# Kernel optimization log

Measured on AMD Instinct MI355X. Metric: run time of the kernel, lower is better.

Reference implementation:

```python
import jax, jax.numpy as jnp
import numpy as np

H = 8      # head count
ES = 96    # per-head dim
EMB = H * ES
L = 6      # layers
B, T = 8, 512
LN_EPS = 1e-5

def _layernorm(x, g, b):
    mu = jnp.mean(x, axis=-1, keepdims=True)
    var = jnp.mean(jnp.square(x - mu), axis=-1, keepdims=True)
    return (x - mu) * jax.lax.rsqrt(var + LN_EPS) * g + b

def setup_inputs() -> dict:
    key = jax.random.key(0)
    ks = jax.random.split(key, 6)
    s = 0.02
    return {
        "x": jax.random.normal(ks[0], (B, T, EMB), jnp.float32),
        "Wkqv": jax.random.normal(ks[1], (L, 3 * ES, ES), jnp.float32) * s,
        "Wproj": jax.random.normal(ks[2], (L, EMB, EMB), jnp.float32) * s,
        "ln1_g": jnp.ones((L, EMB), jnp.float32),
        "ln1_b": jnp.zeros((L, EMB), jnp.float32),
        "ln2_g": jnp.ones((L, EMB), jnp.float32),
        "ln2_b": jnp.zeros((L, EMB), jnp.float32),
        "ff_w1": jax.random.normal(ks[3], (L, 4 * EMB, EMB), jnp.float32) * s,
        "ff_b1": jnp.zeros((L, 4 * EMB), jnp.float32),
        "ff_w2": jax.random.normal(ks[4], (L, EMB, 4 * EMB), jnp.float32) * s,
        "ff_b2": jnp.zeros((L, EMB), jnp.float32),
    }

def _forward(x, Wkqv, Wproj, ln1_g, ln1_b, ln2_g, ln2_b, ff_w1, ff_b1, ff_w2, ff_b2):
    scale = 1.0 / jnp.sqrt(jnp.float32(ES))

    def step(carry, p):
        x, prev = carry
        wkqv, wproj, g1, b1, g2, b2, w1, bb1, w2, bb2 = p
        Bx, Tx, _ = x.shape
        xh = x.reshape(Bx, Tx, H, ES)                         # [B,T,H,es]
        kqv = jnp.einsum('bthe,fe->bthf', xh, wkqv)           # [B,T,H,3es]
        k, q, v = jnp.split(kqv, 3, axis=-1)                  # torch.split order: k,q,v
        # residual attention: raw scores + previous layer's raw scores
        score = jnp.einsum('bihk,bjhk->bijh', q, k) * scale + prev  # [B,T,T,H]
        att = jax.nn.softmax(score, axis=2)                   # over key axis j
        res = jnp.einsum('btih,bihs->bths', att, v).reshape(Bx, Tx, EMB)
        res = res @ wproj.T
        x = _layernorm(x + res, g1, b1)
        ff = jax.nn.gelu(x @ w1.T + bb1, approximate=False) @ w2.T + bb2
        x = _layernorm(x + ff, g2, b2)
        return (x, score), None

    prev0 = jnp.zeros((x.shape[0], x.shape[1], x.shape[1], H), x.dtype)
    (x, _), _ = jax.lax.scan(step, (x, prev0),
                             (Wkqv, Wproj, ln1_g, ln1_b, ln2_g, ln2_b,
                              ff_w1, ff_b1, ff_w2, ff_b2))
    return x

def reference(x, Wkqv, Wproj, ln1_g, ln1_b, ln2_g, ln2_b, ff_w1, ff_b1, ff_w2, ff_b2):
    return _forward(x, Wkqv, Wproj, ln1_g, ln1_b, ln2_g, ln2_b, ff_w1, ff_b1, ff_w2, ff_b2)
```

## Files before the change

kernel.cpp:

```cpp
#include <hip/hip_runtime.h>
#include <math.h>

#define BB 8
#define TT 512
#define HH 8
#define ESS 96
#define EMBD 768
#define FFD 3072
#define NLAYER 6
#define KHMAX 576

typedef unsigned short ushort_t;
typedef __attribute__((ext_vector_type(8))) short short8;
typedef __attribute__((ext_vector_type(4))) float f32x4;
typedef __attribute__((ext_vector_type(4))) unsigned short ushort4v;

static __device__ __forceinline__ ushort_t f2b(float f) {
    unsigned u = __builtin_bit_cast(unsigned, f);
    unsigned r = (u + 0x7fffu + ((u >> 16) & 1u)) >> 16;
    return (ushort_t)r;
}
static __device__ __forceinline__ float b2f(ushort_t u) {
    return __builtin_bit_cast(float, ((unsigned)u) << 16);
}

#define GLDS(gp, lp) __builtin_amdgcn_global_load_lds( \
    (const __attribute__((address_space(1))) void*)(gp), \
    (__attribute__((address_space(3))) void*)(lp), 16, 0, 0)

template<int BM, int BN, int WM, int WN, int OUTBF, int HASBIAS, int GELU, int BETA>
__global__ __launch_bounds__(256) void gemm_mfma(
    const ushort_t* __restrict__ A, int lda,
    const ushort_t* __restrict__ B, int ldb,
    void* __restrict__ Cv, int ldc,
    int K, float alpha,
    const float* __restrict__ bias,
    int bdiv, long sAb, long sAh, long sBb, long sBh, long sCb, long sCh)
{
    constexpr int BK = 32;
    constexpr int WTM = BM / WM;
    constexpr int WTN = BN / WN;
    constexpr int MF = WTM / 16, NF = WTN / 16;
    constexpr int ACH = (BM * BK * 2) / 1024;
    constexpr int BCH = (BN * BK * 2) / 1024;

    const int z = blockIdx.z;
    const int zb = z / bdiv, zh = z % bdiv;
    A += (long)zb * sAb + (long)zh * sAh;
    B += (long)zb * sBb + (long)zh * sBh;
    const long coff = (long)zb * sCb + (long)zh * sCh;

    __shared__ ushort_t As[BM * BK];
    __shared__ ushort_t Bs[BN * BK];

    const int tid = threadIdx.x;
    const int w = tid >> 6, lane = tid & 63;
    const int wr = w / WN, wc = w % WN;
    const int m0 = blockIdx.y * BM;
    const int n0 = blockIdx.x * BN;

    f32x4 acc[MF][NF] = {};

    const int fr = lane & 15;
    const int kb = lane >> 4;

    for (int k0 = 0; k0 < K; k0 += BK) {
#pragma unroll
        for (int q = 0; q < (ACH + 3) / 4; ++q) {
            int ci = q * 4 + w;
            if (ci < ACH) {
                int e = ci * 512 + lane * 8;
                int r = e >> 5, c = e & 31;
                GLDS(A + (long)(m0 + r) * lda + (k0 + c), (char*)As + ci * 1024);
            }
        }
#pragma unroll
        for (int q = 0; q < (BCH + 3) / 4; ++q) {
            int ci = q * 4 + w;
            if (ci < BCH) {
                int e = ci * 512 + lane * 8;
                int r = e >> 5, c = e & 31;
                GLDS(B + (long)(n0 + r) * ldb + (k0 + c), (char*)Bs + ci * 1024);
            }
        }
        __syncthreads();

        short8 af[MF], bfr[NF];
#pragma unroll
        for (int fm = 0; fm < MF; ++fm)
            af[fm] = *(const short8*)&As[(wr * WTM + fm * 16 + fr) * 32 + kb * 8];
#pragma unroll
        for (int fn = 0; fn < NF; ++fn)
            bfr[fn] = *(const short8*)&Bs[(wc * WTN + fn * 16 + fr) * 32 + kb * 8];
#pragma unroll
        for (int fm = 0; fm < MF; ++fm)
#pragma unroll
            for (int fn = 0; fn < NF; ++fn)
                acc[fm][fn] = __builtin_amdgcn_mfma_f32_16x16x32_bf16(
                    af[fm], bfr[fn], acc[fm][fn], 0, 0, 0);
        __syncthreads();
    }

    const int cr = lane >> 4;
    const int cc = lane & 15;
#pragma unroll
    for (int fm = 0; fm < MF; ++fm) {
#pragma unroll
        for (int fn = 0; fn < NF; ++fn) {
#pragma unroll
            for (int j = 0; j < 4; ++j) {
                int gm = m0 + wr * WTM + fm * 16 + cr * 4 + j;
                int gn = n0 + wc * WTN + fn * 16 + cc;
                float v = alpha * acc[fm][fn][j];
                if (HASBIAS) v += bias[gn];
                if (GELU) {
                    float zz = 1.5957691216f * fmaf(0.044715f * v * v, v, v);
                    v = v / (1.f + __expf(-zz));
                }
                long idx = coff + (long)gm * ldc + gn;
                if (BETA) v += ((const float*)Cv)[idx];
                if (OUTBF) ((ushort_t*)Cv)[idx] = f2b(v);
                else       ((float*)Cv)[idx] = v;
            }
        }
    }
}

__global__ __launch_bounds__(256) void kqv_gemm(
    const ushort_t* __restrict__ A,
    const ushort_t* __restrict__ Bw,
    ushort_t* __restrict__ Kh, ushort_t* __restrict__ Qh,
    ushort_t* __restrict__ Vt, int loff, float scale)
{
    constexpr int BM = 128, BN = 96, BK = 32;
    __shared__ ushort_t As[BM * BK];
    __shared__ ushort_t Bs[BN * BK];

    const int tid = threadIdx.x;
    const int w = tid >> 6, lane = tid & 63;
    const int m0 = blockIdx.y * BM;
    const int n0 = blockIdx.x * BN;

    f32x4 acc[2][6] = {};
    const int fr = lane & 15;
    const int kb = lane >> 4;

    for (int k0 = 0; k0 < 96; k0 += BK) {
#pragma unroll
        for (int q = 0; q < 2; ++q) {
            int ci = q * 4 + w;
            int e = ci * 512 + lane * 8;
            int r = e >> 5, c = e & 31;
            GLDS(A + (long)(m0 + r) * ESS + (k0 + c), (char*)As + ci * 1024);
        }
        {
            int ci = w;
            int e = ci * 512 + lane * 8;
            int r = e >> 5, c = e & 31;
            GLDS(Bw + (long)(n0 + r) * ESS + (k0 + c), (char*)Bs + ci * 1024);
            if (w < 2) {
                int ci2 = 4 + w;
                int e2 = ci2 * 512 + lane * 8;
                int r2 = e2 >> 5, c2 = e2 & 31;
                GLDS(Bw + (long)(n0 + r2) * ESS + (k0 + c2), (char*)Bs + ci2 * 1024);
            }
        }
        __syncthreads();

        short8 af[2], bfr[6];
#pragma unroll
        for (int fm = 0; fm < 2; ++fm)
            af[fm] = *(const short8*)&As[(w * 32 + fm * 16 + fr) * 32 + kb * 8];
#pragma unroll
        for (int fn = 0; fn < 6; ++fn)
            bfr[fn] = *(const short8*)&Bs[(fn * 16 + fr) * 32 + kb * 8];
#pragma unroll
        for (int fm = 0; fm < 2; ++fm)
#pragma unroll
            for (int fn = 0; fn < 6; ++fn)
                acc[fm][fn] = __builtin_amdgcn_mfma_f32_16x16x32_bf16(
                    af[fm], bfr[fn], acc[fm][fn], 0, 0, 0);
        __syncthreads();
    }

    const int cr = lane >> 4;
    const int cc = lane & 15;
    const int kind = blockIdx.x;
#pragma unroll
    for (int fm = 0; fm < 2; ++fm) {
#pragma unroll
        for (int fn = 0; fn < 6; ++fn) {
#pragma unroll
            for (int j = 0; j < 4; ++j) {
                int gm = m0 + w * 32 + fm * 16 + cr * 4 + j;
                int s = fn * 16 + cc;
                float v = acc[fm][fn][j];
                int h = gm & 7;
                int bt = gm >> 3;
                int t = bt & 511, b = bt >> 9;
                int bh = b * HH + h;
                if (kind == 0)
                    Kh[((long)(bh * TT + t)) * KHMAX + loff + s] = f2b(v);
                else if (kind == 1)
                    Qh[((long)(bh * TT + t)) * KHMAX + loff + s] = f2b(v * scale);
                else
                    Vt[((long)(bh * ESS + s)) * TT + t] = f2b(v);
            }
        }
    }
}

__global__ __launch_bounds__(256) void fused_attn(
    const ushort_t* __restrict__ Qh,
    const ushort_t* __restrict__ Kh,
    const ushort_t* __restrict__ Vt,
    ushort_t* __restrict__ attn,
    int Kd)
{
    __shared__ char lds[40960];
    ushort_t* As = (ushort_t*)lds;
    ushort_t* Bs = (ushort_t*)(lds + 2048);
    ushort_t* Pt = (ushort_t*)(lds + 2048);
    ushort_t* Vs = (ushort_t*)(lds + 34816);
    float* red   = (float*)(lds + 34816);
    float* red2  = (float*)(lds + 35328);

    const int wg = blockIdx.x;
    const int xcd = wg & 7;
    const int sub = wg >> 3;
    const int m0 = (sub & 15) * 32;
    const int bh = (sub >> 4) * 8 + xcd;
    const int b = bh >> 3, h = bh & 7;

    const int tid = threadIdx.x;
    const int w = tid >> 6, lane = tid & 63;
    const int fr = lane & 15, kb = lane >> 4;
    const int cr = kb, cc = fr;

    f32x4 acc[2][8] = {};

    for (int k0 = 0; k0 < Kd; k0 += 32) {
        if (w < 2) {
            int e = w * 512 + lane * 8;
            int r = e >> 5, c = e & 31;
            GLDS(Qh + ((long)(bh * TT + m0 + r)) * KHMAX + k0 + c,
                 (char*)As + w * 1024);
        }
#pragma unroll
        for (int q = 0; q < 8; ++q) {
            int ci = q * 4 + w;
            int e = ci * 512 + lane * 8;
            int r = e >> 5, c = e & 31;
            GLDS(Kh + ((long)(bh * TT + r)) * KHMAX + k0 + c,
                 (char*)Bs + ci * 1024);
        }
        __syncthreads();
        short8 af0 = *(const short8*)&As[fr * 32 + kb * 8];
        short8 af1 = *(const short8*)&As[(16 + fr) * 32 + kb * 8];
#pragma unroll
        for (int fn = 0; fn < 8; ++fn) {
            short8 bf = *(const short8*)&Bs[(w * 128 + fn * 16 + fr) * 32 + kb * 8];
            acc[0][fn] = __builtin_amdgcn_mfma_f32_16x16x32_bf16(af0, bf, acc[0][fn], 0, 0, 0);
            acc[1][fn] = __builtin_amdgcn_mfma_f32_16x16x32_bf16(af1, bf, acc[1][fn], 0, 0, 0);
        }
        __syncthreads();
    }

#pragma unroll
    for (int fm = 0; fm < 2; ++fm)
#pragma unroll
        for (int j = 0; j < 4; ++j) {
            float mx = -1e30f;
#pragma unroll
            for (int fn = 0; fn < 8; ++fn) mx = fmaxf(mx, acc[fm][fn][j]);
            for (int o = 1; o <= 8; o <<= 1) mx = fmaxf(mx, __shfl_xor(mx, o));
            if (cc == 0) red[w * 32 + fm * 16 + cr * 4 + j] = mx;
        }
    __syncthreads();

    float inv[2][4];
#pragma unroll
    for (int fm = 0; fm < 2; ++fm)
#pragma unroll
        for (int j = 0; j < 4; ++j) {
            int r = fm * 16 + cr * 4 + j;
            float mx = fmaxf(fmaxf(red[r], red[32 + r]), fmaxf(red[64 + r], red[96 + r]));
            float s = 0.f;
#pragma unroll
            for (int fn = 0; fn < 8; ++fn) {
                float e = __expf(acc[fm][fn][j] - mx);
                acc[fm][fn][j] = e;
                s += e;
            }
            for (int o = 1; o <= 8; o <<= 1) s += __shfl_xor(s, o);
            if (cc == 0) red2[w * 32 + r] = s;
        }
    __syncthreads();
#pragma unroll
    for (int fm = 0; fm < 2; ++fm)
#pragma unroll
        for (int j = 0; j < 4; ++j) {
            int r = fm * 16 + cr * 4 + j;
            inv[fm][j] = 1.f / (red2[r] + red2[32 + r] + red2[64 + r] + red2[96 + r]);
        }

#pragma unroll
    for (int fm = 0; fm < 2; ++fm)
#pragma unroll
        for (int fn = 0; fn < 8; ++fn)
#pragma unroll
            for (int j = 0; j < 4; ++j) {
                int row = fm * 16 + cr * 4 + j;
                int col = w * 128 + fn * 16 + cc;
                Pt[row * 512 + (col ^ ((row & 7) << 3))] = f2b(acc[fm][fn][j] * inv[fm][j]);
            }
    __syncthreads();

    const int wr = w >> 1, wc2 = w & 1;
    f32x4 po[3] = {};
    for (int j0 = 0; j0 < TT; j0 += 32) {
#pragma unroll
        for (int q = 0; q < 2; ++q) {
            int ci = q * 4 + w;
            if (ci < 6) {
                int e = ci * 512 + lane * 8;
                int r = e >> 5, c = e & 31;
                GLDS(Vt + ((long)(bh * ESS + r)) * TT + j0 + c, (char*)Vs + ci * 1024);
            }
        }
        __syncthreads();
        int prow = wr * 16 + fr;
        short8 pa = *(const short8*)&Pt[prow * 512 + ((j0 + kb * 8) ^ ((prow & 7) << 3))];
#pragma unroll
        for (int fn = 0; fn < 3; ++fn) {
            short8 vb = *(const short8*)&Vs[(wc2 * 48 + fn * 16 + fr) * 32 + kb * 8];
            po[fn] = __builtin_amdgcn_mfma_f32_16x16x32_bf16(pa, vb, po[fn], 0, 0, 0);
        }
        __syncthreads();
    }

#pragma unroll
    for (int fn = 0; fn < 3; ++fn)
#pragma unroll
        for (int j = 0; j < 4; ++j) {
            int grow = m0 + wr * 16 + cr * 4 + j;
            int gcol = h * ESS + wc2 * 48 + fn * 16 + cc;
            attn[((long)(b * TT + grow)) * EMBD + gcol] = f2b(po[fn][j]);
        }
}

__global__ __launch_bounds__(256) void cvt_f2b(
    const float* __restrict__ in, ushort_t* __restrict__ out)
{
    const int i = blockIdx.x * 256 + threadIdx.x;
    float4 v = ((const float4*)in)[i];
    ushort4v o = {f2b(v.x), f2b(v.y), f2b(v.z), f2b(v.w)};
    ((ushort4v*)out)[i] = o;
}

static __device__ __forceinline__ void cvt_w_one(
    int r, int layer,
    const float* Wkqv, const float* Wproj, const float* w1, const float* w2,
    ushort_t* dst_layer)
{
    const float* src; int base;
    if (r < 6912)        { src = Wkqv  + (long)layer * 27648;   base = 0; }
    else if (r < 154368) { src = Wproj + (long)layer * 589824;  base = 6912; }
    else if (r < 744192) { src = w1    + (long)layer * 2359296; base = 154368; }
    else                 { src = w2    + (long)layer * 2359296; base = 744192; }
    int j = r - base;
    float4 v = ((const float4*)src)[j];
    ushort4v o = {f2b(v.x), f2b(v.y), f2b(v.z), f2b(v.w)};
    ((ushort4v*)dst_layer)[r] = o;
}

__global__ __launch_bounds__(256) void cvt_weights_all(
    const float* __restrict__ Wkqv, const float* __restrict__ Wproj,
    const float* __restrict__ w1, const float* __restrict__ w2,
    ushort_t* __restrict__ dst)
{
    int i4 = blockIdx.x * 256 + threadIdx.x;
    int layer = i4 / 1334016;
    int r = i4 - layer * 1334016;
    cvt_w_one(r, layer, Wkqv, Wproj, w1, w2, dst + (long)layer * 5336064);
}

__global__ __launch_bounds__(256) void cvt_weights_layer(
    const float* __restrict__ Wkqv, const float* __restrict__ Wproj,
    const float* __restrict__ w1, const float* __restrict__ w2,
    ushort_t* __restrict__ dst, int layer)
{
    int r = blockIdx.x * 256 + threadIdx.x;
    cvt_w_one(r, layer, Wkqv, Wproj, w1, w2, dst);
}

__global__ __launch_bounds__(192) void add_ln(
    float* __restrict__ x, const ushort_t* __restrict__ r0,
    const ushort_t* __restrict__ r1, const float* __restrict__ bias,
    const float* __restrict__ g, const float* __restrict__ bta,
    ushort_t* __restrict__ xb)
{
    const long row = blockIdx.x;
    float4* xr = (float4*)(x + row * EMBD);
    const ushort4v* q0 = (const ushort4v*)(r0 + row * EMBD);
    const ushort4v* q1 = (const ushort4v*)(r1 + row * EMBD);
    __shared__ float sh[4];
    const int tid = threadIdx.x;
    const int lane = tid & 63, w = tid >> 6;

    float4 a = xr[tid];
    ushort4v u0 = q0[tid], u1 = q1[tid];
    float v[4] = {a.x + b2f(u0.x) + b2f(u1.x), a.y + b2f(u0.y) + b2f(u1.y),
                  a.z + b2f(u0.z) + b2f(u1.z), a.w + b2f(u0.w) + b2f(u1.w)};
    if (bias) {
        float4 b4 = ((const float4*)bias)[tid];
        v[0] += b4.x; v[1] += b4.y; v[2] += b4.z; v[3] += b4.w;
    }
    float s = v[0] + v[1] + v[2] + v[3];
    for (int o = 32; o; o >>= 1) s += __shfl_xor(s, o);
    if (lane == 0) sh[w] = s;
    __syncthreads();
    float mu = (sh[0] + sh[1] + sh[2]) * (1.f / EMBD);

    float var = 0.f;
#pragma unroll
    for (int c = 0; c < 4; ++c) { float d = v[c] - mu; var += d * d; }
    for (int o = 32; o; o >>= 1) var += __shfl_xor(var, o);
    __syncthreads();
    if (lane == 0) sh[w] = var;
    __syncthreads();
    var = (sh[0] + sh[1] + sh[2]) * (1.f / EMBD);
    float rstd = rsqrtf(var + 1e-5f);

    const float4 g4 = ((const float4*)g)[tid];
    const float4 b4 = ((const float4*)bta)[tid];
    float o0 = (v[0] - mu) * rstd * g4.x + b4.x;
    float o1 = (v[1] - mu) * rstd * g4.y + b4.y;
    float o2 = (v[2] - mu) * rstd * g4.z + b4.z;
    float o3 = (v[3] - mu) * rstd * g4.w + b4.w;
    float4 ov = {o0, o1, o2, o3};
    xr[tid] = ov;
    ushort4v ob = {f2b(o0), f2b(o1), f2b(o2), f2b(o3)};
    ((ushort4v*)(xb + row * EMBD))[tid] = ob;
}

extern "C" void kernel_launch(void* const* d_in, const int* in_sizes, int n_in,
                              void* d_out, int out_size, void* d_ws, size_t ws_size,
                              hipStream_t stream) {
    const float* x_in  = (const float*)d_in[0];
    const float* Wkqv  = (const float*)d_in[1];
    const float* Wproj = (const float*)d_in[2];
    const float* ln1_g = (const float*)d_in[3];
    const float* ln1_b = (const float*)d_in[4];
    const float* ln2_g = (const float*)d_in[5];
    const float* ln2_b = (const float*)d_in[6];
    const float* ff_w1 = (const float*)d_in[7];
    const float* ff_b1 = (const float*)d_in[8];
    const float* ff_w2 = (const float*)d_in[9];
    const float* ff_b2 = (const float*)d_in[10];

    float* x = (float*)d_out;
    char* ws = (char*)d_ws;
    ushort_t* Qh     = (ushort_t*)(ws);
    ushort_t* Kh     = (ushort_t*)(ws + 37748736);
    ushort_t* Vtb    = (ushort_t*)(ws + 75497472);
    ushort_t* res0b  = (ushort_t*)(ws + 75497472);
    ushort_t* res1b  = (ushort_t*)(ws + 81788928);
    ushort_t* h1b    = (ushort_t*)(ws + 100663296);
    ushort_t* xb     = (ushort_t*)(ws + 125829120);
    ushort_t* attnb  = (ushort_t*)(ws + 132120576);
    ushort_t* Wall   = (ushort_t*)(ws + 138412032);
    const size_t WLAYER_B = 10672128;
    const int    WLAYER_E = 5336064;
    const int big = (ws_size >= 138412032 + 6 * WLAYER_B) ? 1 : 0;
    const long RES_STRIDE = 3145728;

    hipMemcpyAsync(x, x_in, (size_t)BB * TT * EMBD * sizeof(float),
                   hipMemcpyDeviceToDevice, stream);
    cvt_f2b<<<3072, 256, 0, stream>>>(x_in, xb);
    if (big)
        cvt_weights_all<<<31266, 256, 0, stream>>>(Wkqv, Wproj, ff_w1, ff_w2, Wall);

    const float scale = 0.10206207261596577f;

    for (int l = 0; l < NLAYER; ++l) {
        const float* b1 = ff_b1 + (size_t)l * FFD;
        const float* b2 = ff_b2 + (size_t)l * EMBD;

        ushort_t* Wl = Wall + (big ? (long)l * WLAYER_E : 0);
        if (!big)
            cvt_weights_layer<<<5211, 256, 0, stream>>>(Wkqv, Wproj, ff_w1, ff_w2, Wl, l);
        ushort_t* Wkqvb  = Wl;
        ushort_t* Wprojb = Wl + 27648;
        ushort_t* W1b    = Wl + 617472;
        ushort_t* W2b    = Wl + 2976768;

        kqv_gemm<<<dim3(3, 256, 1), 256, 0, stream>>>(
            xb, Wkqvb, Kh, Qh, Vtb, l * ESS, scale);

        fused_attn<<<1024, 256, 0, stream>>>(
            Qh, Kh, Vtb, attnb, ESS * (l + 1));

        gemm_mfma<128, 128, 2, 2, 1, 0, 0, 0><<<dim3(6, 32, 2), 256, 0, stream>>>(
            attnb, EMBD, Wprojb, EMBD, res0b, EMBD, EMBD / 2, 1.f, nullptr,
            1, 384, 0, 384, 0, RES_STRIDE, 0);

        add_ln<<<BB * TT, 192, 0, stream>>>(x, res0b, res1b, nullptr,
            ln1_g + (size_t)l * EMBD, ln1_b + (size_t)l * EMBD, xb);

        gemm_mfma<128, 128, 2, 2, 1, 1, 1, 0><<<dim3(24, 32, 1), 256, 0, stream>>>(
            xb, EMBD, W1b, EMBD, h1b, FFD, EMBD, 1.f, b1,
            1, 0, 0, 0, 0, 0, 0);

        gemm_mfma<128, 128, 2, 2, 1, 0, 0, 0><<<dim3(6, 32, 2), 256, 0, stream>>>(
            h1b, FFD, W2b, FFD, res0b, EMBD, FFD / 2, 1.f, nullptr,
            1, 1536, 0, 1536, 0, RES_STRIDE, 0);

        add_ln<<<BB * TT, 192, 0, stream>>>(x, res0b, res1b, b2,
            ln2_g + (size_t)l * EMBD, ln2_b + (size_t)l * EMBD, xb);
    }
}
```

Before: 1.143 ms.

## Pipeline QK^T loop with per-wave K staging and direct Q register loads

The score GEMM in fused_attn now loads Q fragments straight from global memory into registers instead of staging them through LDS. Each wave stages only the K rows it consumes, in two halves, and uses vmcnt/lgkmcnt waits in place of block-wide barriers so the next step's loads overlap the current MFMAs. This removes the two __syncthreads per k-step and the Q LDS buffer. The hand-counted waitcnt values are fragile and could produce races if the compiler emits a different number of memory ops. Q register loads are also less coalesced than before.

Measured after the change: 1.143 ms. Within noise of the previous version (-0.0%).

```diff
diff --git a/kernel.cpp b/kernel.cpp
--- a/kernel.cpp
+++ b/kernel.cpp
@@ -217,13 +217,12 @@
     ushort_t* __restrict__ attn,
     int Kd)
 {
-    __shared__ char lds[40960];
-    ushort_t* As = (ushort_t*)lds;
-    ushort_t* Bs = (ushort_t*)(lds + 2048);
-    ushort_t* Pt = (ushort_t*)(lds + 2048);
-    ushort_t* Vs = (ushort_t*)(lds + 34816);
-    float* red   = (float*)(lds + 34816);
-    float* red2  = (float*)(lds + 35328);
+    __shared__ char lds[38912];
+    ushort_t* Bs = (ushort_t*)lds;
+    ushort_t* Pt = (ushort_t*)lds;
+    ushort_t* Vs = (ushort_t*)(lds + 32768);
+    float* red   = (float*)(lds + 32768);
+    float* red2  = (float*)(lds + 33280);
 
     const int wg = blockIdx.x;
     const int xcd = wg & 7;
@@ -239,32 +238,55 @@
 
     f32x4 acc[2][8] = {};
 
-    for (int k0 = 0; k0 < Kd; k0 += 32) {
-        if (w < 2) {
-            int e = w * 512 + lane * 8;
-            int r = e >> 5, c = e & 31;
-            GLDS(Qh + ((long)(bh * TT + m0 + r)) * KHMAX + k0 + c,
-                 (char*)As + w * 1024);
-        }
-#pragma unroll
-        for (int q = 0; q < 8; ++q) {
-            int ci = q * 4 + w;
-            int e = ci * 512 + lane * 8;
-            int r = e >> 5, c = e & 31;
-            GLDS(Kh + ((long)(bh * TT + r)) * KHMAX + k0 + c,
-                 (char*)Bs + ci * 1024);
-        }
-        __syncthreads();
-        short8 af0 = *(const short8*)&As[fr * 32 + kb * 8];
-        short8 af1 = *(const short8*)&As[(16 + fr) * 32 + kb * 8];
-#pragma unroll
-        for (int fn = 0; fn < 8; ++fn) {
+    const ushort_t* Qbase = Qh + ((long)(bh * TT + m0 + fr)) * KHMAX + kb * 8;
+    const int ci0 = w * 8;
+    const int nsteps = Kd >> 5;
+
+#define STAGE_SUB(s, kk) \
+    _Pragma("unroll") \
+    for (int q = 0; q < 4; ++q) { \
+        int ci = ci0 + (s) * 4 + q; \
+        int e = ci * 512 + lane * 8; \
+        int r = e >> 5, c = e & 31; \
+        GLDS(Kh + ((long)(bh * TT + r)) * KHMAX + (kk) + c, (char*)Bs + ci * 1024); \
+    }
+
+    short8 afc0 = *(const short8*)(Qbase);
+    short8 afc1 = *(const short8*)(Qbase + 16 * KHMAX);
+    STAGE_SUB(0, 0)
+    STAGE_SUB(1, 0)
+
+    for (int i = 0; i < nsteps; ++i) {
+        const int kn = (i + 1 < nsteps) ? (i + 1) * 32 : 0;
+
+        asm volatile("s_waitcnt vmcnt(4)" ::: "memory");
+        __builtin_amdgcn_sched_barrier(0);
+#pragma unroll
+        for (int fn = 0; fn < 4; ++fn) {
             short8 bf = *(const short8*)&Bs[(w * 128 + fn * 16 + fr) * 32 + kb * 8];
-            acc[0][fn] = __builtin_amdgcn_mfma_f32_16x16x32_bf16(af0, bf, acc[0][fn], 0, 0, 0);
-            acc[1][fn] = __builtin_amdgcn_mfma_f32_16x16x32_bf16(af1, bf, acc[1][fn], 0, 0, 0);
-        }
-        __syncthreads();
-    }
+            acc[0][fn] = __builtin_amdgcn_mfma_f32_16x16x32_bf16(afc0, bf, acc[0][fn], 0, 0, 0);
+            acc[1][fn] = __builtin_amdgcn_mfma_f32_16x16x32_bf16(afc1, bf, acc[1][fn], 0, 0, 0);
+        }
+        asm volatile("s_waitcnt lgkmcnt(0)" ::: "memory");
+        __builtin_amdgcn_sched_barrier(0);
+        short8 afn0 = *(const short8*)(Qbase + kn);
+        short8 afn1 = *(const short8*)(Qbase + 16 * KHMAX + kn);
+        STAGE_SUB(0, kn)
+        asm volatile("s_waitcnt vmcnt(6)" ::: "memory");
+        __builtin_amdgcn_sched_barrier(0);
+#pragma unroll
+        for (int fn = 4; fn < 8; ++fn) {
+            short8 bf = *(const short8*)&Bs[(w * 128 + fn * 16 + fr) * 32 + kb * 8];
+            acc[0][fn] = __builtin_amdgcn_mfma_f32_16x16x32_bf16(afc0, bf, acc[0][fn], 0, 0, 0);
+            acc[1][fn] = __builtin_amdgcn_mfma_f32_16x16x32_bf16(afc1, bf, acc[1][fn], 0, 0, 0);
+        }
+        asm volatile("s_waitcnt lgkmcnt(0)" ::: "memory");
+        __builtin_amdgcn_sched_barrier(0);
+        STAGE_SUB(1, kn)
+        afc0 = afn0;
+        afc1 = afn1;
+    }
+#undef STAGE_SUB
 
 #pragma unroll
     for (int fm = 0; fm < 2; ++fm)
```
